# Kernel optimization log

Measured on AMD Instinct MI355X. Metric: run time of the kernel, lower is better.

The kernel has to match this reference:

```python
import jax, jax.numpy as jnp
import numpy as np

N_NODES = 100000
N_EDGES = 3200000


def _sage_conv(x, src, dst, Wl, Wr, b):
    # PyG SAGEConv (aggr='mean', root_weight=True, bias on lin_l):
    # out_i = mean_{j in N(i)} x_j @ Wl + x_i @ Wr + b
    msg = x[src]                                            # [E, F] gather
    s = jax.ops.segment_sum(msg, dst, num_segments=N_NODES)  # [N, F]
    cnt = jax.ops.segment_sum(jnp.ones((src.shape[0], 1), x.dtype), dst,
                              num_segments=N_NODES)          # [N, 1]
    agg = s / jnp.maximum(cnt, 1.0)                          # mean (0 for isolated nodes)
    return agg @ Wl + x @ Wr + b


def setup_inputs() -> dict:
    key = jax.random.key(0)
    ks = jax.random.split(key, 12)
    in_d, hid, out_d = 32, 24, 12
    x = jax.random.normal(ks[0], (N_NODES, in_d), dtype=jnp.float32)
    edge_index = jax.random.randint(ks[1], (2, N_EDGES), 0, N_NODES, dtype=jnp.int64)

    def glorot(k, fan_in, fan_out):
        lim = np.sqrt(6.0 / (fan_in + fan_out)).astype(np.float32)
        return jax.random.uniform(k, (fan_in, fan_out), jnp.float32, -lim, lim)

    return {
        "x": x,
        "edge_index": edge_index,
        "Wl1": glorot(ks[2], in_d, hid), "Wr1": glorot(ks[3], in_d, hid),
        "b1": jnp.zeros((hid,), jnp.float32),
        "Wl2": glorot(ks[4], hid, hid), "Wr2": glorot(ks[5], hid, hid),
        "b2": jnp.zeros((hid,), jnp.float32),
        "Wl3": glorot(ks[6], hid, out_d), "Wr3": glorot(ks[7], hid, out_d),
        "b3": jnp.zeros((out_d,), jnp.float32),
    }


def reference(x, edge_index, Wl1, Wr1, b1, Wl2, Wr2, b2, Wl3, Wr3, b3):
    src, dst = edge_index[0], edge_index[1]
    h = jax.nn.relu(_sage_conv(x, src, dst, Wl1, Wr1, b1))
    h = jax.nn.relu(_sage_conv(h, src, dst, Wl2, Wr2, b2))
    h = jax.nn.sigmoid(_sage_conv(h, src, dst, Wl3, Wr3, b3))
    return h
```

## Files before the change

### kernel.cpp

```cpp
#include <hip/hip_runtime.h>
#include <cstdint>
#include <cstddef>

#define NT 256
constexpr int SHIFT = 7;
constexpr int NBK   = 1024;
constexpr int BMASK = (1 << SHIFT) - 1;
constexpr int EPB   = 12800;

__device__ __forceinline__ float sigf(float v) {
    return 1.0f / (1.0f + __expf(-v));
}
__device__ __forceinline__ float bf2f(unsigned short u) {
    return __uint_as_float((unsigned)u << 16);
}
__device__ __forceinline__ unsigned short f2bf(float f) {
    unsigned u = __float_as_uint(f);
    return (unsigned short)((u + 0x7fffu + ((u >> 16) & 1u)) >> 16);
}


__global__ __launch_bounds__(NT)
void p1_k(const int* __restrict__ dst, int* __restrict__ cnts, int e_total, int nPB)
{
    __shared__ int h[NBK];
    for (int i = threadIdx.x; i < NBK; i += NT) h[i] = 0;
    __syncthreads();
    int base = blockIdx.x * EPB;
    for (int it = 0; it < EPB / NT; ++it) {
        int e = base + it * NT + threadIdx.x;
        if (e < e_total) atomicAdd(&h[dst[e] >> SHIFT], 1);
    }
    __syncthreads();
    for (int b = threadIdx.x; b < NBK; b += NT)
        cnts[b * nPB + blockIdx.x] = h[b];
}

__global__ __launch_bounds__(NT)
void scan1_k(int* data, int* __restrict__ bsum, int n)
{
    __shared__ int s[NT];
    int t = threadIdx.x;
    int i = blockIdx.x * NT + t;
    int v = (i < n) ? data[i] : 0;
    s[t] = v;
    __syncthreads();
    for (int off = 1; off < NT; off <<= 1) {
        int add = (t >= off) ? s[t - off] : 0;
        __syncthreads();
        s[t] += add;
        __syncthreads();
    }
    if (i < n) data[i] = s[t] - v;
    if (t == NT - 1) bsum[blockIdx.x] = s[t];
}

__global__ __launch_bounds__(1024)
void scan2_k(int* bsum, int* __restrict__ boff, int nb)
{
    __shared__ int s[1024];
    int t = threadIdx.x;
    int v = (t < nb) ? bsum[t] : 0;
    s[t] = v;
    __syncthreads();
    for (int off = 1; off < 1024; off <<= 1) {
        int add = (t >= off) ? s[t - off] : 0;
        __syncthreads();
        s[t] += add;
        __syncthreads();
    }
    if (t < nb) boff[t] = s[t] - v;
}

__global__ __launch_bounds__(NT)
void scan3_k(int* data, const int* __restrict__ boff, int n)
{
    int i = blockIdx.x * NT + threadIdx.x;
    if (i < n) data[i] += boff[blockIdx.x];
}

__global__ __launch_bounds__(NT)
void p2_k(const int* __restrict__ src, const int* __restrict__ dst,
          const int* __restrict__ ecnts, unsigned* __restrict__ part,
          int e_total, int nPB)
{
    __shared__ int gb[NBK];
    __shared__ int cur[NBK];
    for (int i = threadIdx.x; i < NBK; i += NT) {
        gb[i]  = ecnts[i * nPB + blockIdx.x];
        cur[i] = 0;
    }
    __syncthreads();
    int base = blockIdx.x * EPB;
    for (int it = 0; it < EPB / NT; ++it) {
        int e = base + it * NT + threadIdx.x;
        if (e < e_total) {
            int d = dst[e];
            int s = src[e];
            int b = d >> SHIFT;
            int r = atomicAdd(&cur[b], 1);
            part[gb[b] + r] = ((unsigned)s << SHIFT) | (unsigned)(d & BMASK);
        }
    }
}

__global__ __launch_bounds__(NT)
void b_k(const unsigned* __restrict__ part, const int* __restrict__ ecnts,
         int* __restrict__ row_ptr, int* __restrict__ col,
         int nPB, int n, int e_total)
{
    constexpr int NPB2 = 1 << SHIFT;
    __shared__ int deg[NT];
    __shared__ int lrp[NT];
    __shared__ int cur[NPB2];
    const int b  = blockIdx.x;
    const int t  = threadIdx.x;
    const int e0 = ecnts[b * nPB];
    const int e1 = (b + 1 < NBK) ? ecnts[(b + 1) * nPB] : e_total;

    deg[t] = 0;
    __syncthreads();
    for (int e = e0 + t; e < e1; e += NT)
        atomicAdd(&deg[part[e] & BMASK], 1);
    __syncthreads();

    int v = deg[t];
    lrp[t] = v;
    __syncthreads();
    for (int off = 1; off < NT; off <<= 1) {
        int add = (t >= off) ? lrp[t - off] : 0;
        __syncthreads();
        lrp[t] += add;
        __syncthreads();
    }
    int excl = lrp[t] - v;
    int node = (b << SHIFT) + t;
    if (t < NPB2 + 1 && node <= n) row_ptr[node] = e0 + excl;
    if (t < NPB2) cur[t] = e0 + excl;
    __syncthreads();

    for (int e = e0 + t; e < e1; e += NT) {
        unsigned p = part[e];
        int pos = atomicAdd(&cur[p & BMASK], 1);
        col[pos] = (int)(p >> SHIFT);
    }
}

__global__ __launch_bounds__(NT)
void cvt_k(const float* __restrict__ x, unsigned short* __restrict__ xb, int ntot)
{
    int i = blockIdx.x * NT + threadIdx.x;
    if (i < ntot) xb[i] = f2bf(x[i]);
}

template<int FIN, int FOUT, int ACT>
__global__ __launch_bounds__(NT)
void gather_k(const unsigned short* __restrict__ Hin, const int* __restrict__ row_ptr,
              const int* __restrict__ col, const float* __restrict__ Wl,
              const float* __restrict__ Wr, const float* __restrict__ b,
              void* __restrict__ Hout, int n)
{
    constexpr int FS  = 32;
    constexpr int NPB = NT / 8;
    constexpr int GS  = 2 * FS + 4;
    __shared__ float sm[NPB * GS];

    const int lane8 = threadIdx.x & 7;
    const int grp   = threadIdx.x >> 3;
    const int node  = blockIdx.x * NPB + grp;
    const bool valid = node < n;

    int rp0 = 0, rp1 = 0;
    if (valid) { rp0 = row_ptr[node]; rp1 = row_ptr[node + 1]; }

    const ushort4* rows = reinterpret_cast<const ushort4*>(Hin);
    float a0 = 0.f, a1 = 0.f, a2 = 0.f, a3 = 0.f;

    if (valid) {
        ushort4 xv = rows[(size_t)node * 8 + lane8];
        int e = rp0;
        for (; e + 3 < rp1; e += 4) {
            int s0 = col[e], s1 = col[e + 1], s2 = col[e + 2], s3 = col[e + 3];
            ushort4 v0 = rows[(size_t)s0 * 8 + lane8];
            ushort4 v1 = rows[(size_t)s1 * 8 + lane8];
            ushort4 v2 = rows[(size_t)s2 * 8 + lane8];
            ushort4 v3 = rows[(size_t)s3 * 8 + lane8];
            a0 += bf2f(v0.x) + bf2f(v1.x) + bf2f(v2.x) + bf2f(v3.x);
            a1 += bf2f(v0.y) + bf2f(v1.y) + bf2f(v2.y) + bf2f(v3.y);
            a2 += bf2f(v0.z) + bf2f(v1.z) + bf2f(v2.z) + bf2f(v3.z);
            a3 += bf2f(v0.w) + bf2f(v1.w) + bf2f(v2.w) + bf2f(v3.w);
        }
        for (; e < rp1; ++e) {
            ushort4 v0 = rows[(size_t)col[e] * 8 + lane8];
            a0 += bf2f(v0.x); a1 += bf2f(v0.y); a2 += bf2f(v0.z); a3 += bf2f(v0.w);
        }
        float invd = 1.0f / fmaxf((float)(rp1 - rp0), 1.0f);
        float* smg = sm + grp * GS;
        smg[4 * lane8 + 0]      = a0 * invd;
        smg[4 * lane8 + 1]      = a1 * invd;
        smg[4 * lane8 + 2]      = a2 * invd;
        smg[4 * lane8 + 3]      = a3 * invd;
        smg[FS + 4 * lane8 + 0] = bf2f(xv.x);
        smg[FS + 4 * lane8 + 1] = bf2f(xv.y);
        smg[FS + 4 * lane8 + 2] = bf2f(xv.z);
        smg[FS + 4 * lane8 + 3] = bf2f(xv.w);
    }
    __syncthreads();

    if (!valid) return;
    const float* smg = sm + grp * GS;

    if constexpr (ACT == 0) {
        unsigned short* out = (unsigned short*)Hout + (size_t)node * FS;
#pragma unroll
        for (int j = 0; j < 4; ++j) {
            int f = lane8 + 8 * j;
            float r = 0.0f;
            if (f < FOUT) {
                float a = b[f];
#pragma unroll
                for (int k = 0; k < FIN; ++k) {
                    a = fmaf(smg[k],      Wl[k * FOUT + f], a);
                    a = fmaf(smg[FS + k], Wr[k * FOUT + f], a);
                }
                r = fmaxf(a, 0.0f);
            }
            out[f] = f2bf(r);
        }
    } else {
        float* out = (float*)Hout + (size_t)node * FOUT;
#pragma unroll
        for (int j = 0; j < (FOUT + 7) / 8; ++j) {
            int f = lane8 + 8 * j;
            if (f < FOUT) {
                float a = b[f];
#pragma unroll
                for (int k = 0; k < FIN; ++k) {
                    a = fmaf(smg[k],      Wl[k * FOUT + f], a);
                    a = fmaf(smg[FS + k], Wr[k * FOUT + f], a);
                }
                out[f] = sigf(a);
            }
        }
    }
}

extern "C" void kernel_launch(void* const* d_in, const int* in_sizes, int n_in,
                              void* d_out, int out_size, void* d_ws, size_t ws_size,
                              hipStream_t stream)
{
    const float* x   = (const float*)d_in[0];
    const int*   ei  = (const int*)d_in[1];
    const float* Wl1 = (const float*)d_in[2];
    const float* Wr1 = (const float*)d_in[3];
    const float* b1  = (const float*)d_in[4];
    const float* Wl2 = (const float*)d_in[5];
    const float* Wr2 = (const float*)d_in[6];
    const float* b2  = (const float*)d_in[7];
    const float* Wl3 = (const float*)d_in[8];
    const float* Wr3 = (const float*)d_in[9];
    const float* b3  = (const float*)d_in[10];

    const int N = in_sizes[0] / 32;
    const int E = in_sizes[1] / 2;
    const int* src = ei;
    const int* dst = ei + E;

    const int nPB = (E + EPB - 1) / EPB;
    const int M   = NBK * nPB;
    const int nSB = (M + NT - 1) / NT;
    const int nBK = ((N - 1) >> SHIFT) + 1;
    const int nbG = (N + 31) / 32;
    const int nbC = (N * 32 + NT - 1) / NT;

    int* row_ptr = (int*)d_ws;
    int* cnts    = row_ptr + (N + 2);
    int* bsum    = cnts + M;
    int* boff    = bsum + 1024;
    int* col     = boff + 1024;
    unsigned* part = (unsigned*)(col + E);
    size_t int_elems = (size_t)(N + 2) + M + 2048 + (size_t)E * 2;
    int_elems = (int_elems + 3) & ~(size_t)3;
    unsigned short* xb  = (unsigned short*)((int*)d_ws + int_elems);
    unsigned short* H1b = xb  + (size_t)N * 32;
    unsigned short* H2b = H1b + (size_t)N * 32;

    p1_k   <<<nPB, NT,   0, stream>>>(dst, cnts, E, nPB);
    scan1_k<<<nSB, NT,   0, stream>>>(cnts, bsum, M);
    scan2_k<<<1,   1024, 0, stream>>>(bsum, boff, nSB);
    scan3_k<<<nSB, NT,   0, stream>>>(cnts, boff, M);
    p2_k   <<<nPB, NT,   0, stream>>>(src, dst, cnts, part, E, nPB);
    b_k    <<<nBK, NT,   0, stream>>>(part, cnts, row_ptr, col, nPB, N, E);

    cvt_k  <<<nbC, NT,   0, stream>>>(x, xb, N * 32);

    gather_k<32, 24, 0><<<nbG, NT, 0, stream>>>(xb,  row_ptr, col, Wl1, Wr1, b1, H1b, N);
    gather_k<24, 24, 0><<<nbG, NT, 0, stream>>>(H1b, row_ptr, col, Wl2, Wr2, b2, H2b, N);
    gather_k<24, 12, 1><<<nbG, NT, 0, stream>>>(H2b, row_ptr, col, Wl3, Wr3, b3, (float*)d_out, N);
}
```

Baseline: 266.6 us.

## Split neighbor gather into two source-range passes and fold scan offset into consumers

Each node's CSR edge list is partitioned by source index (below or above half the node count), and each layer's aggregation runs as two kernels. The first sums neighbours from the lower source half into a float partial buffer, and the second adds the upper half and applies the linear layers. The intent is to shrink the random-gather working set per pass so it fits better in cache (bf16 features of 50k nodes, about 3.2MB per half). The scan3 pass is also removed by adding the block offset inside p2_k and b_k. In exchange, each layer gets an extra launch plus a write and read of an N×32 float partial buffer, and b_k does extra atomics.

```diff
diff --git a/kernel.cpp b/kernel.cpp
--- a/kernel.cpp
+++ b/kernel.cpp
@@ -3,10 +3,11 @@
 #include <cstddef>
 
 #define NT 256
-constexpr int SHIFT = 7;
-constexpr int NBK   = 1024;
-constexpr int BMASK = (1 << SHIFT) - 1;
-constexpr int EPB   = 12800;
+constexpr int SHIFT  = 7;
+constexpr int NBK    = 1024;
+constexpr int BMASK  = (1 << SHIFT) - 1;
+constexpr int EPB    = 12800;
+constexpr int TSPLIT = 50000;
 
 __device__ __forceinline__ float sigf(float v) {
     return 1.0f / (1.0f + __expf(-v));
@@ -73,21 +74,15 @@
 }
 
 __global__ __launch_bounds__(NT)
-void scan3_k(int* data, const int* __restrict__ boff, int n)
-{
-    int i = blockIdx.x * NT + threadIdx.x;
-    if (i < n) data[i] += boff[blockIdx.x];
-}
-
-__global__ __launch_bounds__(NT)
 void p2_k(const int* __restrict__ src, const int* __restrict__ dst,
-          const int* __restrict__ ecnts, unsigned* __restrict__ part,
-          int e_total, int nPB)
+          const int* __restrict__ ecnts, const int* __restrict__ boff,
+          unsigned* __restrict__ part, int e_total, int nPB)
 {
     __shared__ int gb[NBK];
     __shared__ int cur[NBK];
     for (int i = threadIdx.x; i < NBK; i += NT) {
-        gb[i]  = ecnts[i * nPB + blockIdx.x];
+        int g = i * nPB + blockIdx.x;
+        gb[i]  = ecnts[g] + boff[g / NT];
         cur[i] = 0;
     }
     __syncthreads();
@@ -106,43 +101,54 @@
 
 __global__ __launch_bounds__(NT)
 void b_k(const unsigned* __restrict__ part, const int* __restrict__ ecnts,
-         int* __restrict__ row_ptr, int* __restrict__ col,
+         const int* __restrict__ boff, int* __restrict__ row_ptr,
+         int* __restrict__ mptr, int* __restrict__ col,
          int nPB, int n, int e_total)
 {
-    constexpr int NPB2 = 1 << SHIFT;
-    __shared__ int deg[NT];
-    __shared__ int lrp[NT];
-    __shared__ int cur[NPB2];
-    const int b  = blockIdx.x;
-    const int t  = threadIdx.x;
-    const int e0 = ecnts[b * nPB];
-    const int e1 = (b + 1 < NBK) ? ecnts[(b + 1) * nPB] : e_total;
-
-    deg[t] = 0;
-    __syncthreads();
-    for (int e = e0 + t; e < e1; e += NT)
-        atomicAdd(&deg[part[e] & BMASK], 1);
-    __syncthreads();
-
-    int v = deg[t];
-    lrp[t] = v;
-    __syncthreads();
-    for (int off = 1; off < NT; off <<= 1) {
-        int add = (t >= off) ? lrp[t - off] : 0;
-        __syncthreads();
-        lrp[t] += add;
-        __syncthreads();
-    }
-    int excl = lrp[t] - v;
-    int node = (b << SHIFT) + t;
-    if (t < NPB2 + 1 && node <= n) row_ptr[node] = e0 + excl;
-    if (t < NPB2) cur[t] = e0 + excl;
-    __syncthreads();
-
+    constexpr int NB2 = 1 << SHIFT;
+    __shared__ int d0[NB2], dt[NB2], sc[NB2], c0[NB2], c1[NB2];
+    const int b = blockIdx.x;
+    const int t = threadIdx.x;
+    int g0 = b * nPB;
+    const int e0 = ecnts[g0] + boff[g0 / NT];
+    int g1 = (b + 1) * nPB;
+    const int e1 = ecnts[g1] + boff[g1 / NT];
+
+    if (t < NB2) { d0[t] = 0; dt[t] = 0; }
+    __syncthreads();
     for (int e = e0 + t; e < e1; e += NT) {
         unsigned p = part[e];
-        int pos = atomicAdd(&cur[p & BMASK], 1);
-        col[pos] = (int)(p >> SHIFT);
+        int l = p & BMASK;
+        int s = (int)(p >> SHIFT);
+        atomicAdd(&dt[l], 1);
+        if (s < TSPLIT) atomicAdd(&d0[l], 1);
+    }
+    __syncthreads();
+    if (t < NB2) sc[t] = dt[t];
+    __syncthreads();
+    for (int off = 1; off < NB2; off <<= 1) {
+        int add = (t >= off && t < NB2) ? sc[t - off] : 0;
+        __syncthreads();
+        if (t < NB2) sc[t] += add;
+        __syncthreads();
+    }
+    if (t < NB2) {
+        int excl = sc[t] - dt[t];
+        int st0  = e0 + excl;
+        int node = (b << SHIFT) + t;
+        if (node <= n) row_ptr[node] = st0;
+        if (node <  n) mptr[node]    = st0 + d0[t];
+        c0[t] = st0;
+        c1[t] = st0 + d0[t];
+    }
+    __syncthreads();
+    for (int e = e0 + t; e < e1; e += NT) {
+        unsigned p = part[e];
+        int l = p & BMASK;
+        int s = (int)(p >> SHIFT);
+        int* cp = (s < TSPLIT) ? &c0[l] : &c1[l];
+        int pos = atomicAdd(cp, 1);
+        col[pos] = s;
     }
 }
 
@@ -153,12 +159,45 @@
     if (i < ntot) xb[i] = f2bf(x[i]);
 }
 
+__global__ __launch_bounds__(NT)
+void gA_k(const unsigned short* __restrict__ Hin, const int* __restrict__ row_ptr,
+          const int* __restrict__ mptr, const int* __restrict__ col,
+          float* __restrict__ P, int n)
+{
+    const int lane8 = threadIdx.x & 7;
+    const int grp   = threadIdx.x >> 3;
+    const int node  = blockIdx.x * (NT / 8) + grp;
+    if (node >= n) return;
+    const int e0 = row_ptr[node];
+    const int e1 = mptr[node];
+    const ushort4* rows = reinterpret_cast<const ushort4*>(Hin);
+    float a0 = 0.f, a1 = 0.f, a2 = 0.f, a3 = 0.f;
+    int e = e0;
+    for (; e + 3 < e1; e += 4) {
+        int s0 = col[e], s1 = col[e + 1], s2 = col[e + 2], s3 = col[e + 3];
+        ushort4 v0 = rows[(size_t)s0 * 8 + lane8];
+        ushort4 v1 = rows[(size_t)s1 * 8 + lane8];
+        ushort4 v2 = rows[(size_t)s2 * 8 + lane8];
+        ushort4 v3 = rows[(size_t)s3 * 8 + lane8];
+        a0 += bf2f(v0.x) + bf2f(v1.x) + bf2f(v2.x) + bf2f(v3.x);
+        a1 += bf2f(v0.y) + bf2f(v1.y) + bf2f(v2.y) + bf2f(v3.y);
+        a2 += bf2f(v0.z) + bf2f(v1.z) + bf2f(v2.z) + bf2f(v3.z);
+        a3 += bf2f(v0.w) + bf2f(v1.w) + bf2f(v2.w) + bf2f(v3.w);
+    }
+    for (; e < e1; ++e) {
+        ushort4 v0 = rows[(size_t)col[e] * 8 + lane8];
+        a0 += bf2f(v0.x); a1 += bf2f(v0.y); a2 += bf2f(v0.z); a3 += bf2f(v0.w);
+    }
+    reinterpret_cast<float4*>(P + (size_t)node * 32)[lane8] = make_float4(a0, a1, a2, a3);
+}
+
 template<int FIN, int FOUT, int ACT>
 __global__ __launch_bounds__(NT)
-void gather_k(const unsigned short* __restrict__ Hin, const int* __restrict__ row_ptr,
-              const int* __restrict__ col, const float* __restrict__ Wl,
-              const float* __restrict__ Wr, const float* __restrict__ b,
-              void* __restrict__ Hout, int n)
+void gB_k(const unsigned short* __restrict__ Hin, const int* __restrict__ row_ptr,
+          const int* __restrict__ mptr, const int* __restrict__ col,
+          const float* __restrict__ P, const float* __restrict__ Wl,
+          const float* __restrict__ Wr, const float* __restrict__ b,
+          void* __restrict__ Hout, int n)
 {
     constexpr int FS  = 32;
     constexpr int NPB = NT / 8;
@@ -170,15 +209,15 @@
     const int node  = blockIdx.x * NPB + grp;
     const bool valid = node < n;
 
-    int rp0 = 0, rp1 = 0;
-    if (valid) { rp0 = row_ptr[node]; rp1 = row_ptr[node + 1]; }
-
-    const ushort4* rows = reinterpret_cast<const ushort4*>(Hin);
-    float a0 = 0.f, a1 = 0.f, a2 = 0.f, a3 = 0.f;
-
     if (valid) {
+        const int rp0 = row_ptr[node];
+        const int rpm = mptr[node];
+        const int rp1 = row_ptr[node + 1];
+        const ushort4* rows = reinterpret_cast<const ushort4*>(Hin);
+        float4 pv = reinterpret_cast<const float4*>(P + (size_t)node * 32)[lane8];
+        float a0 = pv.x, a1 = pv.y, a2 = pv.z, a3 = pv.w;
         ushort4 xv = rows[(size_t)node * 8 + lane8];
-        int e = rp0;
+        int e = rpm;
         for (; e + 3 < rp1; e += 4) {
             int s0 = col[e], s1 = col[e + 1], s2 = col[e + 2], s3 = col[e + 3];
             ushort4 v0 = rows[(size_t)s0 * 8 + lane8];
@@ -277,24 +316,30 @@
     int* cnts    = row_ptr + (N + 2);
     int* bsum    = cnts + M;
     int* boff    = bsum + 1024;
-    int* col     = boff + 1024;
-    unsigned* part = (unsigned*)(col + E);
-    size_t int_elems = (size_t)(N + 2) + M + 2048 + (size_t)E * 2;
-    int_elems = (int_elems + 3) & ~(size_t)3;
-    unsigned short* xb  = (unsigned short*)((int*)d_ws + int_elems);
+    int* mptr    = boff + 1024;
+    size_t off   = (size_t)(N + 2) + M + 2048 + N;
+    off = (off + 3) & ~(size_t)3;
+    int* col     = (int*)d_ws + off;
+    off += E;
+    unsigned* part = (unsigned*)((int*)d_ws + off);
+    float*    P    = (float*)part;
+    off += E;
+    unsigned short* xb  = (unsigned short*)((int*)d_ws + off);
     unsigned short* H1b = xb  + (size_t)N * 32;
     unsigned short* H2b = H1b + (size_t)N * 32;
 
     p1_k   <<<nPB, NT,   0, stream>>>(dst, cnts, E, nPB);
     scan1_k<<<nSB, NT,   0, stream>>>(cnts, bsum, M);
     scan2_k<<<1,   1024, 0, stream>>>(bsum, boff, nSB);
-    scan3_k<<<nSB, NT,   0, stream>>>(cnts, boff, M);
-    p2_k   <<<nPB, NT,   0, stream>>>(src, dst, cnts, part, E, nPB);
-    b_k    <<<nBK, NT,   0, stream>>>(part, cnts, row_ptr, col, nPB, N, E);
+    p2_k   <<<nPB, NT,   0, stream>>>(src, dst, cnts, boff, part, E, nPB);
+    b_k    <<<nBK, NT,   0, stream>>>(part, cnts, boff, row_ptr, mptr, col, nPB, N, E);
 
     cvt_k  <<<nbC, NT,   0, stream>>>(x, xb, N * 32);
 
-    gather_k<32, 24, 0><<<nbG, NT, 0, stream>>>(xb,  row_ptr, col, Wl1, Wr1, b1, H1b, N);
-    gather_k<24, 24, 0><<<nbG, NT, 0, stream>>>(H1b, row_ptr, col, Wl2, Wr2, b2, H2b, N);
-    gather_k<24, 12, 1><<<nbG, NT, 0, stream>>>(H2b, row_ptr, col, Wl3, Wr3, b3, (float*)d_out, N);
-}
+    gA_k            <<<nbG, NT, 0, stream>>>(xb,  row_ptr, mptr, col, P, N);
+    gB_k<32, 24, 0> <<<nbG, NT, 0, stream>>>(xb,  row_ptr, mptr, col, P, Wl1, Wr1, b1, H1b, N);
+    gA_k            <<<nbG, NT, 0, stream>>>(H1b, row_ptr, mptr, col, P, N);
+    gB_k<24, 24, 0> <<<nbG, NT, 0, stream>>>(H1b, row_ptr, mptr, col, P, Wl2, Wr2, b2, H2b, N);
+    gA_k            <<<nbG, NT, 0, stream>>>(H2b, row_ptr, mptr, col, P, N);
+    gB_k<24, 12, 1> <<<nbG, NT, 0, stream>>>(H2b, row_ptr, mptr, col, P, Wl3, Wr3, b3, (float*)d_out, N);
+}
```

Result: no change. 263.3 us (-1.2%).
